# Performance work log

Hardware: AMD Instinct MI355X
Metric: run time of the kernel (lower is better)

Reference implementation:

```python
import jax, jax.numpy as jnp
import numpy as np

N, E, D, H, K = 8192, 8, 1024, 4096, 2


def setup_inputs() -> dict:
    key = jax.random.key(0)
    ks = jax.random.split(key, 12)
    s = 0.02  # init scale for weights
    return {
        "x": jax.random.normal(ks[0], (N, D), jnp.float32),
        "noise": jax.random.normal(ks[1], (N, E), jnp.float32),
        "Wg_w": jax.random.normal(ks[2], (D, E), jnp.float32) * s,
        "Wg_b": jnp.zeros((E,), jnp.float32),
        "Wn_w": jax.random.normal(ks[3], (D, E), jnp.float32) * s,
        "Wn_b": jnp.zeros((E,), jnp.float32),
        "w1": jax.random.normal(ks[4], (E, D, H), jnp.float32) * s,
        "b1": jnp.zeros((E, H), jnp.float32),
        "w2": jax.random.normal(ks[5], (E, H, D), jnp.float32) * s,
        "b2": jnp.zeros((E, D), jnp.float32),
        "k": K,
    }


def reference(x, noise, Wg_w, Wg_b, Wn_w, Wn_b, w1, b1, w2, b2, k):
    # --- noisy top-k gating: H(x) = Wg(x) + noise * softplus(Wn(x)) ---
    g_logits = x @ Wg_w + Wg_b                       # [N, E]
    n_scale = jax.nn.softplus(x @ Wn_w + Wn_b)       # [N, E]
    h = g_logits + noise * n_scale                   # [N, E]
    topk_vals, topk_inds = jax.lax.top_k(h, k)       # [N, k]
    gates = jax.nn.softmax(topk_vals, axis=-1)       # [N, k]

    # Scatter top-k gates into a dense [N, E] map (zeros for unselected experts),
    # so the weighted combine is exactly sum_j gates[n,j] * expert_{inds[n,j]}(x_n).
    n_tok, n_exp = h.shape
    dense_gates = jnp.zeros((n_tok, n_exp), h.dtype).at[
        jnp.arange(n_tok)[:, None], topk_inds
    ].set(gates)                                     # [N, E]

    # --- per-expert 2-layer MLP: fc2(relu(fc1(x))) ---
    hid = jax.nn.relu(jnp.einsum('nd,edh->neh', x, w1) + b1)  # [N, E, H]
    y = jnp.einsum('neh,ehd->ned', hid, w2) + b2              # [N, E, D]
    out = jnp.einsum('ned,ne->nd', y, dense_gates)            # [N, D]
    return out
```

## Files before the change

kernel.cpp:

```cpp
#include <hip/hip_runtime.h>
#include <hip/hip_bf16.h>

#define NTOK 8192
#define NEXP 8
#define DMODEL 1024
#define DHID 4096

typedef __bf16 bf16x8 __attribute__((ext_vector_type(8)));
typedef float f32x4 __attribute__((ext_vector_type(4)));

__device__ __forceinline__ unsigned short f2bf(float f) {
  return __builtin_bit_cast(unsigned short, __float2bfloat16(f));
}

__device__ __forceinline__ void gload_lds16(const void* g, void* l) {
  __builtin_amdgcn_global_load_lds(
      (const __attribute__((address_space(1))) unsigned int*)g,
      (__attribute__((address_space(3))) unsigned int*)l, 16, 0, 0);
}

__device__ __forceinline__ int imin(int a, int b) { return a < b ? a : b; }

constexpr size_t OFF_XB   = 0;
constexpr size_t OFF_W1T  = OFF_XB + (size_t)NTOK * DMODEL * 2;
constexpr size_t OFF_W2T  = OFF_W1T + (size_t)NEXP * DHID * DMODEL * 2;
constexpr size_t OFF_HID  = OFF_W2T + (size_t)NEXP * DMODEL * DHID * 2;
constexpr size_t OFF_IDX  = OFF_HID + (size_t)NTOK * 2 * DHID * 2;
constexpr size_t OFF_GATE = OFF_IDX + (size_t)NTOK * 2 * 4;
constexpr size_t OFF_LIST = OFF_GATE + (size_t)NTOK * 2 * 4;
constexpr size_t OFF_CNT  = OFF_LIST + (size_t)NTOK * 2 * 4;
constexpr size_t OFF_OFFS = OFF_CNT + 128;
constexpr size_t OFF_CUR  = OFF_OFFS + 128;

__global__ void transpose_bf16_kernel(const float* __restrict__ in,
                                      unsigned short* __restrict__ out,
                                      int R, int C) {
  __shared__ float sh[64][65];
  const size_t ebase = (size_t)blockIdx.z * R * C;
  const float* ine = in + ebase;
  unsigned short* oute = out + ebase;
  int c0 = blockIdx.x * 64, r0 = blockIdx.y * 64;
  int tx = threadIdx.x & 15, ty = threadIdx.x >> 4;
#pragma unroll
  for (int p = 0; p < 4; ++p) {
    int row = ty + p * 16;
    float4 v = *(const float4*)&ine[(size_t)(r0 + row) * C + c0 + tx * 4];
    sh[row][tx * 4 + 0] = v.x;
    sh[row][tx * 4 + 1] = v.y;
    sh[row][tx * 4 + 2] = v.z;
    sh[row][tx * 4 + 3] = v.w;
  }
  __syncthreads();
#pragma unroll
  for (int p = 0; p < 4; ++p) {
    int crow = ty + p * 16;
    ushort4 o;
    o.x = f2bf(sh[tx * 4 + 0][crow]);
    o.y = f2bf(sh[tx * 4 + 1][crow]);
    o.z = f2bf(sh[tx * 4 + 2][crow]);
    o.w = f2bf(sh[tx * 4 + 3][crow]);
    *(ushort4*)&oute[(size_t)(c0 + crow) * R + r0 + tx * 4] = o;
  }
}

__global__ void gating_kernel(const float* __restrict__ x,
                              const float* __restrict__ noise,
                              const float* __restrict__ Wg_w,
                              const float* __restrict__ Wg_b,
                              const float* __restrict__ Wn_w,
                              const float* __restrict__ Wn_b,
                              unsigned short* __restrict__ xb,
                              int* __restrict__ topk_idx,
                              float* __restrict__ topk_gate,
                              int* __restrict__ counts) {
  int wave = threadIdx.x >> 6;
  int lane = threadIdx.x & 63;
  int n = blockIdx.x * 4 + wave;
  if (n >= NTOK) return;

  float ag[8] = {0.f, 0.f, 0.f, 0.f, 0.f, 0.f, 0.f, 0.f};
  float an[8] = {0.f, 0.f, 0.f, 0.f, 0.f, 0.f, 0.f, 0.f};
  const float* xr = x + (size_t)n * DMODEL;
  unsigned short* xbr = xb + (size_t)n * DMODEL;
#pragma unroll 4
  for (int i = 0; i < DMODEL / 64; ++i) {
    int d = lane + i * 64;
    float xv = xr[d];
    xbr[d] = f2bf(xv);
    const float4* wg = (const float4*)(Wg_w + (size_t)d * 8);
    const float4* wn = (const float4*)(Wn_w + (size_t)d * 8);
    float4 g0 = wg[0], g1 = wg[1];
    float4 n0 = wn[0], n1 = wn[1];
    ag[0] += xv * g0.x; ag[1] += xv * g0.y; ag[2] += xv * g0.z; ag[3] += xv * g0.w;
    ag[4] += xv * g1.x; ag[5] += xv * g1.y; ag[6] += xv * g1.z; ag[7] += xv * g1.w;
    an[0] += xv * n0.x; an[1] += xv * n0.y; an[2] += xv * n0.z; an[3] += xv * n0.w;
    an[4] += xv * n1.x; an[5] += xv * n1.y; an[6] += xv * n1.z; an[7] += xv * n1.w;
  }
#pragma unroll
  for (int off = 32; off > 0; off >>= 1) {
#pragma unroll
    for (int j = 0; j < 8; ++j) {
      ag[j] += __shfl_down(ag[j], off, 64);
      an[j] += __shfl_down(an[j], off, 64);
    }
  }
  if (lane == 0) {
    float h[8];
#pragma unroll
    for (int e = 0; e < 8; ++e) {
      float gl = ag[e] + Wg_b[e];
      float z = an[e] + Wn_b[e];
      float sp = fmaxf(z, 0.f) + log1pf(expf(-fabsf(z)));
      h[e] = gl + noise[(size_t)n * 8 + e] * sp;
    }
    int i0 = 0; float v0 = h[0];
#pragma unroll
    for (int e = 1; e < 8; ++e)
      if (h[e] > v0) { v0 = h[e]; i0 = e; }
    int i1 = -1; float v1 = -1e30f;
#pragma unroll
    for (int e = 0; e < 8; ++e)
      if (e != i0 && h[e] > v1) { v1 = h[e]; i1 = e; }
    float e1 = expf(v1 - v0);
    float inv = 1.f / (1.f + e1);
    topk_idx[n * 2] = i0;
    topk_idx[n * 2 + 1] = i1;
    topk_gate[n * 2] = inv;
    topk_gate[n * 2 + 1] = e1 * inv;
    atomicAdd(&counts[i0], 1);
    atomicAdd(&counts[i1], 1);
  }
}

__global__ void scan_kernel(const int* __restrict__ counts,
                            int* __restrict__ offsets, int* __restrict__ cursor) {
  if (threadIdx.x == 0) {
    int acc = 0;
    for (int e = 0; e < NEXP; ++e) {
      offsets[e] = acc;
      cursor[e] = acc;
      acc += counts[e];
    }
    offsets[NEXP] = acc;
  }
}

__global__ void scatter_kernel(const int* __restrict__ topk_idx,
                               int* __restrict__ cursor, int* __restrict__ list) {
  int n = blockIdx.x * 256 + threadIdx.x;
  if (n >= NTOK) return;
#pragma unroll
  for (int j = 0; j < 2; ++j) {
    int e = topk_idx[n * 2 + j];
    int pos = atomicAdd(&cursor[e], 1);
    list[pos] = n * 2 + j;
  }
}

#define VMW(N) asm volatile("s_waitcnt vmcnt(" #N ")" ::: "memory")

template <int MODE>
__global__ __launch_bounds__(256) void expert_gemm(
    const unsigned short* __restrict__ Asrc, const unsigned short* __restrict__ Bt,
    const float* __restrict__ bias, const int* __restrict__ offsets,
    const int* __restrict__ list, const float* __restrict__ gates,
    unsigned short* __restrict__ hid, float* __restrict__ out) {
  constexpr int K = MODE ? DHID : DMODEL;
  constexpr int Nout = MODE ? DMODEL : DHID;
  constexpr int NT = K / 32;

  const int gx = gridDim.x;
  const int lin = blockIdx.x + gx * (blockIdx.y + 64 * blockIdx.z);
  const int e = lin & 7;
  const int r = lin >> 3;
  const int by = r & 63;
  const int bx = r >> 6;

  const int off = offsets[e];
  const int ne = offsets[e + 1] - off;
  const int m0 = by * 128;
  if (m0 >= ne) return;
  const int n0 = bx * 128;

  __shared__ alignas(16) unsigned short Al[3][128 * 32];
  __shared__ alignas(16) unsigned short Bl[3][128 * 32];

  const int tid = threadIdx.x;
  const int lane = tid & 63;
  const int w = tid >> 6;
  const int wm = (w >> 1) * 64;
  const int wn = (w & 1) * 64;
  const int lr = lane & 15;
  const int kg = lane >> 4;
  const int chrd = (kg ^ ((lr >> 1) & 3)) * 8;

  const unsigned short* srcA[2];
  const unsigned short* srcB[2];
#pragma unroll
  for (int i = 0; i < 2; ++i) {
    int q = tid + i * 256;
    int rr = q >> 2, c = q & 3;
    int cs = c ^ ((rr >> 1) & 3);
    int p = off + imin(m0 + rr, ne - 1);
    if (MODE == 0) {
      int token = list[p] >> 1;
      srcA[i] = Asrc + (size_t)token * DMODEL + cs * 8;
    } else {
      srcA[i] = Asrc + (size_t)p * DHID + cs * 8;
    }
    srcB[i] = Bt + (size_t)e * Nout * K + (size_t)(n0 + rr) * K + cs * 8;
  }

  f32x4 acc[4][4] = {};

  auto stage = [&](int slot, int kt) {
#pragma unroll
    for (int i = 0; i < 2; ++i) {
      int q = tid + i * 256;
      gload_lds16(srcA[i] + kt * 32, &Al[slot][q * 8]);
      gload_lds16(srcB[i] + kt * 32, &Bl[slot][q * 8]);
    }
  };

  auto compute = [&](int slot) {
    bf16x8 af[4], bfr[4];
#pragma unroll
    for (int mf = 0; mf < 4; ++mf)
      af[mf] = *(const bf16x8*)&Al[slot][(wm + mf * 16 + lr) * 32 + chrd];
#pragma unroll
    for (int nf = 0; nf < 4; ++nf)
      bfr[nf] = *(const bf16x8*)&Bl[slot][(wn + nf * 16 + lr) * 32 + chrd];
    asm volatile("s_waitcnt lgkmcnt(0)" ::: "memory");
    __builtin_amdgcn_sched_barrier(0);
#pragma unroll
    for (int mf = 0; mf < 4; ++mf)
#pragma unroll
      for (int nf = 0; nf < 4; ++nf)
        acc[mf][nf] = __builtin_amdgcn_mfma_f32_16x16x32_bf16(af[mf], bfr[nf],
                                                              acc[mf][nf], 0, 0, 0);
  };

  stage(0, 0);
  stage(1, 1);
  stage(2, 2);

  int cur = 0;
  for (int t = 0; t < NT; ++t) {
    if (t < NT - 2) { VMW(8); }
    else if (t == NT - 2) { VMW(4); }
    else { VMW(0); }
    __builtin_amdgcn_s_barrier();
    __builtin_amdgcn_sched_barrier(0);
    compute(cur);
    asm volatile("s_waitcnt lgkmcnt(0)" ::: "memory");
    __builtin_amdgcn_sched_barrier(0);
    __builtin_amdgcn_s_barrier();
    if (t + 3 < NT) stage(cur, t + 3);
    cur = (cur == 2) ? 0 : cur + 1;
  }

  if (MODE == 0) {
#pragma unroll
    for (int mf = 0; mf < 4; ++mf) {
#pragma unroll
      for (int j = 0; j < 4; ++j) {
        int rloc = wm + mf * 16 + kg * 4 + j;
        int row = m0 + rloc;
        if (row < ne) {
          size_t p = (size_t)(off + row);
#pragma unroll
          for (int nf = 0; nf < 4; ++nf) {
            int col = n0 + wn + nf * 16 + lr;
            float v = acc[mf][nf][j] + bias[(size_t)e * Nout + col];
            hid[p * DHID + col] = f2bf(fmaxf(v, 0.f));
          }
        }
      }
    }
  } else {
#pragma unroll
    for (int mf = 0; mf < 4; ++mf) {
#pragma unroll
      for (int j = 0; j < 4; ++j) {
        int rloc = wm + mf * 16 + kg * 4 + j;
        int row = m0 + rloc;
        if (row < ne) {
          int lv = list[off + row];
          int token = lv >> 1;
          float g = gates[lv];
#pragma unroll
          for (int nf = 0; nf < 4; ++nf) {
            int col = n0 + wn + nf * 16 + lr;
            float v = (acc[mf][nf][j] + bias[(size_t)e * Nout + col]) * g;
            atomicAdd(&out[(size_t)token * DMODEL + col], v);
          }
        }
      }
    }
  }
}

extern "C" void kernel_launch(void* const* d_in, const int* in_sizes, int n_in,
                              void* d_out, int out_size, void* d_ws, size_t ws_size,
                              hipStream_t stream) {
  const float* x = (const float*)d_in[0];
  const float* noise = (const float*)d_in[1];
  const float* Wg_w = (const float*)d_in[2];
  const float* Wg_b = (const float*)d_in[3];
  const float* Wn_w = (const float*)d_in[4];
  const float* Wn_b = (const float*)d_in[5];
  const float* w1 = (const float*)d_in[6];
  const float* b1 = (const float*)d_in[7];
  const float* w2 = (const float*)d_in[8];
  const float* b2 = (const float*)d_in[9];
  float* out = (float*)d_out;

  char* ws = (char*)d_ws;
  unsigned short* xb = (unsigned short*)(ws + OFF_XB);
  unsigned short* w1t = (unsigned short*)(ws + OFF_W1T);
  unsigned short* w2t = (unsigned short*)(ws + OFF_W2T);
  unsigned short* hid = (unsigned short*)(ws + OFF_HID);
  int* topk_idx = (int*)(ws + OFF_IDX);
  float* topk_gate = (float*)(ws + OFF_GATE);
  int* list = (int*)(ws + OFF_LIST);
  int* counts = (int*)(ws + OFF_CNT);
  int* offsets = (int*)(ws + OFF_OFFS);
  int* cursor = (int*)(ws + OFF_CUR);

  hipMemsetAsync(out, 0, (size_t)NTOK * DMODEL * sizeof(float), stream);
  hipMemsetAsync(counts, 0, NEXP * sizeof(int), stream);

  transpose_bf16_kernel<<<dim3(DHID / 64, DMODEL / 64, NEXP), 256, 0, stream>>>(
      w1, w1t, DMODEL, DHID);
  transpose_bf16_kernel<<<dim3(DMODEL / 64, DHID / 64, NEXP), 256, 0, stream>>>(
      w2, w2t, DHID, DMODEL);

  gating_kernel<<<NTOK / 4, 256, 0, stream>>>(x, noise, Wg_w, Wg_b, Wn_w, Wn_b,
                                              xb, topk_idx, topk_gate, counts);
  scan_kernel<<<1, 64, 0, stream>>>(counts, offsets, cursor);
  scatter_kernel<<<NTOK / 256, 256, 0, stream>>>(topk_idx, cursor, list);

  expert_gemm<0><<<dim3(DHID / 128, 64, NEXP), 256, 0, stream>>>(
      xb, w1t, b1, offsets, list, topk_gate, hid, nullptr);
  expert_gemm<1><<<dim3(DMODEL / 128, 64, NEXP), 256, 0, stream>>>(
      hid, w2t, b2, offsets, list, topk_gate, nullptr, out);
}
```

Measured before the change: 864.6 us.

## Add split-K for second expert GEMM and swizzle block order for L2 reuse

The down-projection GEMM now splits its 4096-long reduction into four 1024-wide chunks, each handled by a separate block, and the partial results are accumulated into the output with the existing atomics. Bias is added only by the first chunk. The first GEMM's block index is remapped into 8x8 super-tiles with a serpentine order so neighbouring blocks share A and B tiles in cache. Splitting K raises the number of blocks for the small-N second GEMM, at the cost of four times as many atomic adds to the output.

Measured after the change: 949.4 us. 9.8% more time.

```diff
diff --git a/kernel.cpp b/kernel.cpp
--- a/kernel.cpp
+++ b/kernel.cpp
@@ -165,16 +165,32 @@
     const float* __restrict__ bias, const int* __restrict__ offsets,
     const int* __restrict__ list, const float* __restrict__ gates,
     unsigned short* __restrict__ hid, float* __restrict__ out) {
-  constexpr int K = MODE ? DHID : DMODEL;
+  constexpr int Krow = MODE ? DHID : DMODEL;
   constexpr int Nout = MODE ? DMODEL : DHID;
-  constexpr int NT = K / 32;
-
-  const int gx = gridDim.x;
-  const int lin = blockIdx.x + gx * (blockIdx.y + 64 * blockIdx.z);
+  constexpr int NT = 32;
+
+  const int gx = gridDim.x, gy = gridDim.y;
+  const int lin = blockIdx.x + gx * (blockIdx.y + gy * blockIdx.z);
   const int e = lin & 7;
-  const int r = lin >> 3;
-  const int by = r & 63;
-  const int bx = r >> 6;
+  int r = lin >> 3;
+
+  int by, bx, kc = 0;
+  if (MODE == 0) {
+    int st = r >> 6;
+    int inner = r & 63;
+    int sm = st >> 2, sn = st & 3;
+    if (sm & 1) sn = 3 - sn;
+    by = sm * 8 + (inner >> 3);
+    bx = sn * 8 + (inner & 7);
+  } else {
+    kc = r >> 9;
+    int r2 = r & 511;
+    int sm = r2 >> 6;
+    int inner = r2 & 63;
+    by = sm * 8 + (inner >> 3);
+    bx = inner & 7;
+  }
+  const int koff = kc * 1024;
 
   const int off = offsets[e];
   const int ne = offsets[e + 1] - off;
@@ -206,9 +222,9 @@
       int token = list[p] >> 1;
       srcA[i] = Asrc + (size_t)token * DMODEL + cs * 8;
     } else {
-      srcA[i] = Asrc + (size_t)p * DHID + cs * 8;
-    }
-    srcB[i] = Bt + (size_t)e * Nout * K + (size_t)(n0 + rr) * K + cs * 8;
+      srcA[i] = Asrc + (size_t)p * DHID + koff + cs * 8;
+    }
+    srcB[i] = Bt + (size_t)e * Nout * Krow + (size_t)(n0 + rr) * Krow + koff + cs * 8;
   }
 
   f32x4 acc[4][4] = {};
@@ -291,7 +307,8 @@
 #pragma unroll
           for (int nf = 0; nf < 4; ++nf) {
             int col = n0 + wn + nf * 16 + lr;
-            float v = (acc[mf][nf][j] + bias[(size_t)e * Nout + col]) * g;
+            float b = (kc == 0) ? bias[(size_t)e * Nout + col] : 0.f;
+            float v = (acc[mf][nf][j] + b) * g;
             atomicAdd(&out[(size_t)token * DMODEL + col], v);
           }
         }
@@ -340,8 +357,8 @@
   scan_kernel<<<1, 64, 0, stream>>>(counts, offsets, cursor);
   scatter_kernel<<<NTOK / 256, 256, 0, stream>>>(topk_idx, cursor, list);
 
-  expert_gemm<0><<<dim3(DHID / 128, 64, NEXP), 256, 0, stream>>>(
+  expert_gemm<0><<<dim3(32, 64, NEXP), 256, 0, stream>>>(
       xb, w1t, b1, offsets, list, topk_gate, hid, nullptr);
-  expert_gemm<1><<<dim3(DMODEL / 128, 64, NEXP), 256, 0, stream>>>(
+  expert_gemm<1><<<dim3(8, 256, NEXP), 256, 0, stream>>>(
       hid, w2t, b2, offsets, list, topk_gate, nullptr, out);
 }
```
